# Optimization experiments

Measured on AMD Instinct MI355X. Metric: run time of the kernel, lower is better.

Reference implementation:

```python
import jax, jax.numpy as jnp
import numpy as np

GRID = 32
N = GRID * GRID
KTOP = 256          # max off-diagonal points kept per diagram (rest are diagonal, zero cost)
SINK_ITERS = 150
_idx = np.arange(N).reshape(GRID, GRID)
_EU = np.concatenate([_idx[:, :-1].ravel(), _idx[:-1, :].ravel()]).astype(np.int32)
_EV = np.concatenate([_idx[:, 1:].ravel(), _idx[1:, :].ravel()]).astype(np.int32)
E = _EU.shape[0]  # 1984 grid edges (4-connectivity, V-construction cubical complex)


def _h0_pairs(v):
    """0-dim persistence pairs of the sublevel filtration of pixel values v [N].
    Kruskal/union-find with the elder rule; trivial edges emit diagonal (w, w) pairs."""
    eu, ev = jnp.asarray(_EU), jnp.asarray(_EV)
    w = jnp.maximum(v[eu], v[ev])
    order = jnp.argsort(w)

    @jax.checkpoint
    def step(state, edge):
        parent, birth = state
        u, vv, wgt = edge
        for _ in range(10):              # pointer jumping: full compression (2^10 >= N)
            parent = parent[parent]
        ru, rv = parent[u], parent[vv]
        bu, bv = birth[ru], birth[rv]
        merge = ru != rv
        u_older = bu <= bv
        older = jnp.where(u_older, ru, rv)
        younger = jnp.where(u_older, rv, ru)
        pb = jnp.where(merge, jnp.maximum(bu, bv), wgt)   # younger component dies
        parent = parent.at[younger].set(jnp.where(merge, older, younger))
        birth = birth.at[older].set(jnp.minimum(bu, bv))
        return (parent, birth), (pb, wgt)

    init = (jnp.arange(N, dtype=jnp.int32), v)
    _, (bs, ds) = jax.lax.scan(step, init, (eu[order], ev[order], w[order]))
    return bs, ds


def _diagrams(img):
    """img [GRID,GRID] -> (b0, d0, b1, d1), each [KTOP]. H1 via superlevel H0 duality."""
    v = img.reshape(-1)
    b0, d0 = _h0_pairs(v)
    b0 = jnp.concatenate([b0, v.min()[None]])   # essential H0 class: (min, max)
    d0 = jnp.concatenate([d0, v.max()[None]])
    nb, nd = _h0_pairs(-v)                       # superlevel-set H0 (essential dropped)
    b1, d1 = -nd, -nb

    def topk(b, d):
        _, i = jax.lax.top_k(d - b, KTOP)        # keep most persistent points
        return b[i], d[i]

    return (*topk(b0, d0), *topk(b1, d1))


def _wasserstein(ab, ad, bb, bd):
    """Entropic 1-Wasserstein between diagrams with L-inf ground metric and diagonal slots."""
    K = ab.shape[0]
    Pa = jnp.stack([ab, ad], -1)
    Pb = jnp.stack([bb, bd], -1)
    Mpp = jnp.max(jnp.abs(Pa[:, None, :] - Pb[None, :, :]), -1)  # [K,K]
    da = 0.5 * (ad - ab)                       # L-inf distance of a-points to diagonal
    db = 0.5 * (bd - bb)
    C = jnp.block([[Mpp, jnp.broadcast_to(da[:, None], (K, K))],
                   [jnp.broadcast_to(db[None, :], (K, K)), jnp.zeros((K, K), ab.dtype)]])
    eps = 0.02 * jnp.maximum(jnp.max(C), 1e-6)

    def it(_, fg):
        f, g = fg
        f = -eps * jax.nn.logsumexp((g[None, :] - C) / eps, axis=1)
        g = -eps * jax.nn.logsumexp((f[:, None] - C) / eps, axis=0)
        return f, g

    f, g = jax.lax.fori_loop(0, SINK_ITERS, it, (jnp.zeros(2 * K), jnp.zeros(2 * K)))
    P = jnp.exp((f[:, None] + g[None, :] - C) / eps)
    return jnp.sum(P * C)


def setup_inputs() -> dict:
    key = jax.random.key(0)
    kx, ky = jax.random.split(key)
    x = jax.random.normal(kx, (4, 4, 256, 256), dtype=jnp.float32)
    y = jax.random.randint(ky, (4, 1, 256, 256), 0, 4)
    return {"x": x, "y": y}


def reference(x, y):
    B, C, H, W = x.shape
    x = jax.nn.softmax(x, axis=1)                               # apply_nonlin
    y_oh = (y == jnp.arange(C)[None, :, None, None]).astype(x.dtype)  # scatter_ one-hot
    kh, kw = H // GRID, W // GRID

    def pool(t):  # adaptive_avg_pool2d to (32, 32)
        b, c = t.shape[:2]
        return t.reshape(b, c, GRID, kh, GRID, kw).mean((3, 5))

    mx = pool(x[:, 1:]).reshape(-1, GRID, GRID)  # drop background channel
    my = pool(y_oh[:, 1:]).reshape(-1, GRID, GRID)
    dx = jax.vmap(_diagrams)(mx)
    dy = jax.vmap(_diagrams)(my)
    w0 = jax.vmap(_wasserstein)(dx[0], dx[1], dy[0], dy[1])
    w1 = jax.vmap(_wasserstein)(dx[2], dx[3], dy[2], dy[3])
    return (jnp.sum(w0) + jnp.sum(w1)) / B
```

## Files before the change

kernel.cpp:

```cpp
#include <hip/hip_runtime.h>
#include <cmath>

#define NPIX 1024
#define NEDGE 1984
#define NPAD 2048
#define KTOP 256
#define NITER 150

typedef __attribute__((ext_vector_type(8))) short bf16x8_t;
typedef __attribute__((ext_vector_type(4))) float f32x4_t;

__device__ __forceinline__ unsigned bf_rne(float x) {
    unsigned b = __float_as_uint(x);
    return (b + 0x7fffu + ((b >> 16) & 1u)) >> 16;
}
__device__ __forceinline__ float rcpf(float x) { return __builtin_amdgcn_rcpf(x); }

template<int CTRL>
__device__ __forceinline__ float dppf(float x) {
    return __int_as_float(__builtin_amdgcn_update_dpp(
        __float_as_int(x), __float_as_int(x), CTRL, 0xF, 0xF, false));
}
__device__ __forceinline__ void wave_red2(float& s, float& m) {
    s += dppf<0x121>(s); m = fminf(m, dppf<0x121>(m));
    s += dppf<0x122>(s); m = fminf(m, dppf<0x122>(m));
    s += dppf<0x124>(s); m = fminf(m, dppf<0x124>(m));
    s += dppf<0x128>(s); m = fminf(m, dppf<0x128>(m));
    s += __int_as_float(__builtin_amdgcn_ds_swizzle(__float_as_int(s), 0x401F));
    m = fminf(m, __int_as_float(__builtin_amdgcn_ds_swizzle(__float_as_int(m), 0x401F)));
    float s0 = __int_as_float(__builtin_amdgcn_readlane(__float_as_int(s), 0));
    float s1 = __int_as_float(__builtin_amdgcn_readlane(__float_as_int(s), 32));
    s = s0 + s1;
    float m0 = __int_as_float(__builtin_amdgcn_readlane(__float_as_int(m), 0));
    float m1 = __int_as_float(__builtin_amdgcn_readlane(__float_as_int(m), 32));
    m = fminf(m0, m1);
}

__device__ __forceinline__ float min8v(const float* a) {
    float4 x0 = *(const float4*)a, x1 = *(const float4*)(a + 4);
    return fminf(fminf(fminf(x0.x, x0.y), fminf(x0.z, x0.w)),
                 fminf(fminf(x1.x, x1.y), fminf(x1.z, x1.w)));
}
__device__ __forceinline__ float sum8v(const float* a) {
    float4 x0 = *(const float4*)a, x1 = *(const float4*)(a + 4);
    return ((x0.x + x0.y) + (x0.z + x0.w)) + ((x1.x + x1.y) + (x1.z + x1.w));
}

__global__ __launch_bounds__(256) void pool_kernel(const float* __restrict__ x,
                                                   const int* __restrict__ y,
                                                   float* __restrict__ pooled) {
    int blk = blockIdx.x;
    int img = blk >> 2;
    int cell = ((blk & 3) << 8) | threadIdx.x;
    int gi = cell >> 5, gj = cell & 31;
    const float L2E = 1.4426950408889634f;
    float acc = 0.f;
    if (img < 12) {
        int b = img / 3, c = img % 3 + 1;
        const float* xb = x + (size_t)b * 262144 + (size_t)gi * 2048 + gj * 8;
        for (int pi = 0; pi < 8; ++pi) {
            const float* xr = xb + pi * 256;
            #pragma unroll
            for (int ph = 0; ph < 2; ++ph) {
                float4 c0 = *(const float4*)(xr + ph * 4);
                float4 c1 = *(const float4*)(xr + ph * 4 + 65536);
                float4 c2 = *(const float4*)(xr + ph * 4 + 131072);
                float4 c3 = *(const float4*)(xr + ph * 4 + 196608);
                const float* f0 = (const float*)&c0;
                const float* f1 = (const float*)&c1;
                const float* f2 = (const float*)&c2;
                const float* f3 = (const float*)&c3;
                #pragma unroll
                for (int k = 0; k < 4; ++k) {
                    float e0 = exp2f(f0[k] * L2E), e1 = exp2f(f1[k] * L2E);
                    float e2 = exp2f(f2[k] * L2E), e3 = exp2f(f3[k] * L2E);
                    float ec = (c == 1) ? e1 : (c == 2) ? e2 : e3;
                    acc += ec / (e0 + e1 + e2 + e3);
                }
            }
        }
    } else {
        int tt = img - 12;
        int b = tt / 3, c = tt % 3 + 1;
        const int* yb = y + (size_t)b * 65536 + (size_t)gi * 2048 + gj * 8;
        int cnt = 0;
        for (int pi = 0; pi < 8; ++pi) {
            const int* yr = yb + pi * 256;
            #pragma unroll
            for (int pj = 0; pj < 8; ++pj) cnt += (yr[pj] == c) ? 1 : 0;
        }
        acc = (float)cnt;
    }
    pooled[img * NPIX + cell] = acc * (1.f / 64.f);
}

__device__ __forceinline__ void cex(unsigned long long& a, unsigned long long& b, bool up) {
    if ((a > b) == up) { unsigned long long t = a; a = b; b = t; }
}
__device__ void bitonic2048_reg(unsigned long long* keys, int tid, bool asc) {
    int i0 = tid << 2;
    for (int k = 2; k <= NPAD; k <<= 1) {
        for (int j = k >> 1; j >= 4; j >>= 1) {
            #pragma unroll
            for (int rep = 0; rep < 4; ++rep) {
                int ii = tid + rep * 512;
                int l = ii ^ j;
                if (l > ii) {
                    unsigned long long a = keys[ii], b = keys[l];
                    bool up = (((ii & k) == 0) == asc);
                    if ((a > b) == up) { keys[ii] = b; keys[l] = a; }
                }
            }
            __syncthreads();
        }
        unsigned long long e0 = keys[i0], e1 = keys[i0 + 1], e2 = keys[i0 + 2], e3 = keys[i0 + 3];
        bool upq = (((i0 & k) == 0) == asc);
        if (k >= 4) {
            cex(e0, e2, upq); cex(e1, e3, upq);
            cex(e0, e1, upq); cex(e2, e3, upq);
        } else {
            cex(e0, e1, asc);
            cex(e2, e3, !asc);
        }
        keys[i0] = e0; keys[i0 + 1] = e1; keys[i0 + 2] = e2; keys[i0 + 3] = e3;
        __syncthreads();
    }
}

__global__ __launch_bounds__(512) void diag_kernel(const float* __restrict__ pooled,
                                                   float* __restrict__ diag) {
    __shared__ float v_[NPIX];
    __shared__ unsigned long long keys[NPAD];
    __shared__ unsigned long long PB[NPIX];
    __shared__ unsigned euv[NPAD];
    __shared__ unsigned long long pbd[NEDGE];
    __shared__ unsigned long long snap[516];
    __shared__ unsigned long long clist[516];
    __shared__ unsigned long long smask[8];
    __shared__ unsigned claimA[NPIX];
    __shared__ unsigned histAll[2048];
    __shared__ float redA[8], redB[8];
    __shared__ float svmin, svmax;
    __shared__ unsigned long long s_prefix, s_T;
    __shared__ unsigned s_need, s_done, s_outcnt, s_ncon;

    int run = blockIdx.x;
    int img = run >> 1, filt = run & 1;
    int tid = threadIdx.x;
    int wv = tid >> 6;
    const float* m = pooled + img * NPIX;

    for (int i = tid; i < NPIX; i += 512) {
        float val = m[i];
        v_[i] = filt ? -val : val;
    }
    __syncthreads();
    float mn = INFINITY, mx = -INFINITY;
    for (int i = tid; i < NPIX; i += 512) { float vv = v_[i]; mn = fminf(mn, vv); mx = fmaxf(mx, vv); }
    for (int o = 32; o; o >>= 1) { mn = fminf(mn, __shfl_xor(mn, o)); mx = fmaxf(mx, __shfl_xor(mx, o)); }
    if ((tid & 63) == 0) { redA[wv] = mn; redB[wv] = mx; }
    __syncthreads();
    if (tid == 0) {
        float a = INFINITY, b = -INFINITY;
        for (int i2 = 0; i2 < 8; ++i2) { a = fminf(a, redA[i2]); b = fmaxf(b, redB[i2]); }
        svmin = a; svmax = b;
    }
    for (int e = tid; e < NPAD; e += 512) {
        unsigned long long key;
        unsigned uv = 0;
        if (e < NEDGE) {
            int u, vv;
            if (e < 992) { int r = e / 31; u = e + r; vv = u + 1; }
            else         { u = e - 992;   vv = u + 32; }
            float w = fmaxf(v_[u], v_[vv]);
            unsigned int bw = __float_as_uint(w);
            bw = (bw & 0x80000000u) ? ~bw : (bw | 0x80000000u);
            key = ((unsigned long long)bw << 11) | (unsigned int)e;
            uv = (unsigned)u | ((unsigned)vv << 16);
        } else key = ~0ULL;
        keys[e] = key;
        euv[e] = uv;
    }
    for (int i = tid; i < NPIX; i += 512)
        PB[i] = ((unsigned long long)__float_as_uint(v_[i]) << 32) | (unsigned)i;
    __syncthreads();
    bitonic2048_reg(keys, tid, true);

    unsigned* PBlo = (unsigned*)PB;
    for (int base = 0; base < NEDGE; base += 512) {
        for (int i = tid; i < NPIX; i += 512) claimA[i] = 0u;
        if (base) {
            for (int rd = 0; rd < 4; ++rd) {
                for (int i = tid; i < NPIX; i += 512) {
                    unsigned pp = PBlo[2 * i];
                    unsigned gg = PBlo[2 * pp];
                    PBlo[2 * i] = gg;
                }
            }
        }
        __syncthreads();
        int bend = (base + 512 < NEDGE) ? base + 512 : NEDGE;
        int bcnt = bend - base;
        bool pend = false;
        if (tid < bcnt) {
            int kk = base + tid;
            unsigned long long key = keys[kk];
            int e = (int)(key & 2047ULL);
            unsigned bw = (unsigned)(key >> 11);
            unsigned uv = euv[e];
            int ra = (int)(uv & 0xffffu), rb = (int)(uv >> 16);
            unsigned pp = PBlo[2 * ra];
            while (pp != (unsigned)ra) { ra = (int)pp; pp = PBlo[2 * ra]; }
            unsigned p2 = PBlo[2 * rb];
            while (p2 != (unsigned)rb) { rb = (int)p2; p2 = PBlo[2 * rb]; }
            if (ra == rb) {
                unsigned wb = (bw & 0x80000000u) ? (bw & 0x7fffffffu) : ~bw;
                pbd[kk] = (unsigned long long)wb | ((unsigned long long)wb << 32);
                snap[tid] = 0ULL;
            } else {
                snap[tid] = ((unsigned long long)bw << 22)
                          | ((unsigned)(ra + 1) << 11) | (unsigned)(rb + 1);
                unsigned tg = (1u << 12) | (unsigned)(511 - tid);
                atomicMax(&claimA[ra], tg);
                atomicMax(&claimA[rb], tg);
                pend = true;
            }
        }
        __syncthreads();
        for (int rnd = 0; rnd < 3; ++rnd) {
            if (pend) {
                unsigned long long sc = snap[tid];
                int ra = (int)((sc >> 11) & 0x7FFu) - 1;
                int rb = (int)(sc & 0x7FFu) - 1;
                unsigned tg = ((unsigned)(rnd + 1) << 12) | (unsigned)(511 - tid);
                if (claimA[ra] == tg && claimA[rb] == tg) {
                    unsigned ob = (unsigned)(sc >> 22);
                    float w = __uint_as_float((ob & 0x80000000u) ? (ob & 0x7fffffffu) : ~ob);
                    float bu = v_[ra], bv = v_[rb];
                    bool uo = (bu <= bv);
                    int older = uo ? ra : rb;
                    int younger = uo ? rb : ra;
                    PBlo[2 * younger] = (unsigned)older;
                    float pb_ = fmaxf(bu, bv);
                    pbd[base + tid] = (unsigned long long)__float_as_uint(pb_)
                                    | ((unsigned long long)__float_as_uint(w) << 32);
                    snap[tid] = 0ULL;
                    pend = false;
                }
            }
            __syncthreads();
            if (rnd < 2) {
                if (pend) {
                    unsigned long long sc = snap[tid];
                    int ra = (int)((sc >> 11) & 0x7FFu) - 1;
                    int rb = (int)(sc & 0x7FFu) - 1;
                    unsigned pp = PBlo[2 * ra];
                    while (pp != (unsigned)ra) { ra = (int)pp; pp = PBlo[2 * ra]; }
                    unsigned p2 = PBlo[2 * rb];
                    while (p2 != (unsigned)rb) { rb = (int)p2; p2 = PBlo[2 * rb]; }
                    if (ra == rb) {
                        unsigned ob = (unsigned)(sc >> 22);
                        unsigned wb2 = (ob & 0x80000000u) ? (ob & 0x7fffffffu) : ~ob;
                        pbd[base + tid] = (unsigned long long)wb2
                                        | ((unsigned long long)wb2 << 32);
                        snap[tid] = 0ULL;
                        pend = false;
                    } else {
                        snap[tid] = (sc & ~0x3FFFFFULL)
                                  | ((unsigned)(ra + 1) << 11) | (unsigned)(rb + 1);
                        unsigned tg = ((unsigned)(rnd + 2) << 12) | (unsigned)(511 - tid);
                        atomicMax(&claimA[ra], tg);
                        atomicMax(&claimA[rb], tg);
                    }
                }
                __syncthreads();
            }
        }
        unsigned long long bmask = __ballot(pend);
        if ((tid & 63) == 0) smask[wv] = bmask;
        __syncthreads();
        if (pend) {
            int lane = tid & 63;
            int pos = __popcll(bmask & ((1ULL << lane) - 1ULL));
            for (int w2 = 0; w2 < wv; ++w2) pos += __popcll(smask[w2]);
            clist[pos] = snap[tid] | ((unsigned long long)tid << 54);
        }
        if (tid == 0) {
            unsigned n = 0;
            for (int w2 = 0; w2 < 8; ++w2) n += (unsigned)__popcll(smask[w2]);
            s_ncon = n;
            clist[n] = 0ULL;
        }
        __syncthreads();
        if (tid == 0) {
            int n = (int)s_ncon;
            unsigned long long sc = clist[0];
            for (int i = 0; i < n; ++i) {
                unsigned long long sn = clist[i + 1];
                int slot = (int)(sc >> 54);
                unsigned ob = (unsigned)((sc >> 22) & 0xFFFFFFFFu);
                float w = __uint_as_float((ob & 0x80000000u) ? (ob & 0x7fffffffu) : ~ob);
                int a = (int)((sc >> 11) & 0x7FFu) - 1;
                int b = (int)(sc & 0x7FFu) - 1;
                unsigned long long qa = PB[a], qb = PB[b];
                int pa = (int)(unsigned)qa, pb = (int)(unsigned)qb;
                while (pa != a || pb != b) {
                    if (pa != a) {
                        unsigned long long na = PB[pa];
                        int ga = (int)(unsigned)na;
                        PBlo[2 * a] = (unsigned)ga;
                        a = pa; pa = ga; qa = na;
                    }
                    if (pb != b) {
                        unsigned long long nb = PB[pb];
                        int gb = (int)(unsigned)nb;
                        PBlo[2 * b] = (unsigned)gb;
                        b = pb; pb = gb; qb = nb;
                    }
                }
                float pb_, pd_;
                if (a != b) {
                    float bu = __uint_as_float((unsigned)(qa >> 32));
                    float bv = __uint_as_float((unsigned)(qb >> 32));
                    bool uo = (bu <= bv);
                    int older = uo ? a : b;
                    int younger = uo ? b : a;
                    pb_ = fmaxf(bu, bv); pd_ = w;
                    PBlo[2 * younger] = (unsigned)older;
                } else { pb_ = w; pd_ = w; }
                pbd[base + slot] = (unsigned long long)__float_as_uint(pb_)
                                 | ((unsigned long long)__float_as_uint(pd_) << 32);
                sc = sn;
            }
        }
        __syncthreads();
    }

    int count = filt ? NEDGE : (NEDGE + 1);
    for (int k = tid; k < NPAD; k += 512) {
        unsigned long long key = 0ULL;
        if (k < count) {
            float pers;
            if (k < NEDGE) {
                unsigned long long pd2 = pbd[k];
                pers = __uint_as_float((unsigned)(pd2 >> 32)) - __uint_as_float((unsigned)pd2);
            } else pers = svmax - svmin;
            key = ((unsigned long long)__float_as_uint(pers) << 32) | (unsigned int)(2047 - k);
        }
        keys[k] = key;
    }
    if (tid == 0) { s_prefix = 0ULL; s_T = 0ULL; s_need = KTOP; s_done = 0; s_outcnt = 0; }
    __syncthreads();

    for (int rnd = 0; rnd < 8; ++rnd) {
        for (int i = tid; i < 2048; i += 512) histAll[i] = 0;
        __syncthreads();
        if (!s_done) {
            int shift = 56 - 8 * rnd;
            unsigned long long pref = s_prefix;
            for (int k = tid; k < NPAD; k += 512) {
                unsigned long long key = keys[k];
                bool act = (rnd == 0) || ((key >> (shift + 8)) == (pref >> (shift + 8)));
                if (act) atomicAdd(&histAll[wv * 256 + (unsigned)((key >> shift) & 255ULL)], 1u);
            }
        }
        __syncthreads();
        if (wv == 0) {
            if (!s_done) {
                int l64 = tid;
                int shift = 56 - 8 * rnd;
                unsigned c0 = 0, c1 = 0, c2 = 0, c3 = 0;
                #pragma unroll
                for (int cp = 0; cp < 8; ++cp) {
                    const unsigned* h = histAll + cp * 256 + 4 * l64;
                    c0 += h[0]; c1 += h[1]; c2 += h[2]; c3 += h[3];
                }
                unsigned s3 = c3, s2 = c2 + s3, s1 = c1 + s2, s0 = c0 + s1;
                unsigned acc2 = s0;
                #pragma unroll
                for (int o = 1; o < 64; o <<= 1) {
                    unsigned v2 = __shfl_down(acc2, o);
                    if (l64 + o < 64) acc2 += v2;
                }
                unsigned above = acc2 - s0;
                unsigned Sn[5] = {above + s0, above + s1, above + s2, above + s3, above};
                unsigned need = s_need;
                #pragma unroll
                for (int q2 = 0; q2 < 4; ++q2) {
                    if (Sn[q2] >= need && Sn[q2 + 1] < need) {
                        unsigned bstar = 4 * l64 + q2;
                        if (Sn[q2] == need) {
                            s_T = s_prefix | ((unsigned long long)bstar << shift);
                            s_done = 1;
                        } else {
                            s_prefix = s_prefix | ((unsigned long long)bstar << shift);
                            s_need = need - Sn[q2 + 1];
                        }
                    }
                }
            }
        }
        __syncthreads();
    }

    {
        unsigned long long T = s_T;
        for (int k = tid; k < NPAD; k += 512) {
            unsigned long long key = keys[k];
            if (key >= T && key != 0ULL) {
                int pos = (int)atomicAdd(&s_outcnt, 1u);
                int kk = 2047 - (int)(key & 0xffffffffULL);
                float b_, d_;
                if (kk < NEDGE) {
                    unsigned long long pd2 = pbd[kk];
                    b_ = __uint_as_float((unsigned)pd2);
                    d_ = __uint_as_float((unsigned)(pd2 >> 32));
                } else { b_ = svmin; d_ = svmax; }
                float ob, od;
                if (!filt) { ob = b_;  od = d_;  }
                else       { ob = -d_; od = -b_; }
                diag[((img * 4) + filt * 2 + 0) * KTOP + pos] = ob;
                diag[((img * 4) + filt * 2 + 1) * KTOP + pos] = od;
            }
        }
    }
}

__global__ __launch_bounds__(512) void sink_kernel(const float* __restrict__ diag,
                                                   float* __restrict__ wres) {
    __shared__ float2 sPA[KTOP], sPB[KTOP];
    __shared__ float sda[KTOP], sdb[KTOP];
    __shared__ float swa[KTOP], swb[KTOP];
    __shared__ __align__(16) unsigned ug_bf[128];
    __shared__ __align__(16) unsigned uf_bf[128];
    __shared__ __align__(16) float uf32[KTOP], ug32[KTOP];
    __shared__ __align__(16) float minF[8], accTF[8], minG[8], accTG[8];
    __shared__ __align__(16) float pm[8];
    __shared__ float s_sig, s_invsig;

    int p = blockIdx.x;
    int img = p % 12, dim = p / 12;
    int t = threadIdx.x;
    int lane = t & 63, w = t >> 6;
    int lr = lane & 15, lg = lane >> 4;
    int r = t >> 1, q = t & 1, jb = q * 128;

    const float* ab  = diag + ((img * 4) + dim * 2) * KTOP;
    const float* ad  = ab + KTOP;
    const float* bbp = diag + (((12 + img) * 4) + dim * 2) * KTOP;
    const float* bdp = bbp + KTOP;

    if (t < KTOP) {
        float a0 = ab[t], a1 = ad[t];
        float b0 = bbp[t], b1 = bdp[t];
        sPA[t] = make_float2(a0, a1);
        sPB[t] = make_float2(b0, b1);
        sda[t] = 0.5f * (a1 - a0);
        sdb[t] = 0.5f * (b1 - b0);
    }
    if (t < 128) ug_bf[t] = 0x3F803F80u;
    __syncthreads();

    {
        float2 A = sPA[r];
        float lmax = 0.f;
        for (int jj = 0; jj < 128; ++jj) {
            float2 B = sPB[jb + jj];
            lmax = fmaxf(lmax, fmaxf(fabsf(A.x - B.x), fabsf(A.y - B.y)));
        }
        if (t < KTOP) lmax = fmaxf(lmax, fmaxf(sda[t], sdb[t]));
        for (int o = 32; o; o >>= 1) lmax = fmaxf(lmax, __shfl_xor(lmax, o));
        if (lane == 0) pm[w] = lmax;
    }
    __syncthreads();
    if (t == 0) {
        float mc = 0.f;
        for (int i = 0; i < 8; ++i) mc = fmaxf(mc, pm[i]);
        float eps = 0.02f * fmaxf(mc, 1e-6f);
        s_sig = 1.4426950408889634f / eps;
        s_invsig = eps * 0.6931471805599453f;
    }
    __syncthreads();
    {
        float sig = s_sig;
        if (t < KTOP) {
            float2 a2 = sPA[t], b2 = sPB[t];
            sPA[t] = make_float2(a2.x * sig, a2.y * sig);
            sPB[t] = make_float2(b2.x * sig, b2.y * sig);
            float da2 = sda[t] * sig, db2 = sdb[t] * sig;
            sda[t] = da2; sdb[t] = db2;
            swa[t] = exp2f(-da2); swb[t] = exp2f(-db2);
        }
    }
    __syncthreads();

    bf16x8_t KfA0[8], KfA1[8], KgA0[8], KgA1[8];
    {
        float2 Af0 = sPA[w * 32 + lr];
        float2 Af1 = sPA[w * 32 + 16 + lr];
        float2 Bg0 = sPB[w * 32 + lr];
        float2 Bg1 = sPB[w * 32 + 16 + lr];
        #pragma unroll
        for (int ks = 0; ks < 8; ++ks) {
            #pragma unroll
            for (int jj = 0; jj < 8; ++jj) {
                int b = ks * 32 + lg * 8 + jj;
                float2 Pb = sPB[b];
                KfA0[ks][jj] = (short)bf_rne(exp2f(-fmaxf(fabsf(Af0.x - Pb.x), fabsf(Af0.y - Pb.y))));
                KfA1[ks][jj] = (short)bf_rne(exp2f(-fmaxf(fabsf(Af1.x - Pb.x), fabsf(Af1.y - Pb.y))));
                float2 Pa = sPA[b];
                KgA0[ks][jj] = (short)bf_rne(exp2f(-fmaxf(fabsf(Pa.x - Bg0.x), fabsf(Pa.y - Bg0.y))));
                KgA1[ks][jj] = (short)bf_rne(exp2f(-fmaxf(fabsf(Pa.x - Bg1.x), fabsf(Pa.y - Bg1.y))));
            }
        }
    }
    float wa0[4], wa1[4], wb0[4], wb1[4];
    #pragma unroll
    for (int g2 = 0; g2 < 4; ++g2) {
        wa0[g2] = swa[w * 32 + lg * 4 + g2];
        wa1[g2] = swa[w * 32 + 16 + lg * 4 + g2];
        wb0[g2] = swb[w * 32 + lg * 4 + g2];
        wb1[g2] = swb[w * 32 + 16 + lg * 4 + g2];
    }

    float cg = 1.f, cf = 1.f, uG2s = 1.f, uF2s = 1.f;
    f32x4_t ugs0 = {1.f, 1.f, 1.f, 1.f}, ugs1 = {1.f, 1.f, 1.f, 1.f};
    f32x4_t ufs0 = {0.f, 0.f, 0.f, 0.f}, ufs1 = {0.f, 0.f, 0.f, 0.f};

    for (int it = 0; it < NITER; ++it) {
        if (it) {
            cg = min8v(minG);
            uG2s = rcpf(cf * (sum8v(accTG) + 256.f * uF2s));
        }
        {
            bf16x8_t Bf[8];
            #pragma unroll
            for (int ks = 0; ks < 8; ++ks) Bf[ks] = ((const bf16x8_t*)ug_bf)[ks * 4 + lg];
            f32x4_t a0 = {0.f, 0.f, 0.f, 0.f}, a1 = {0.f, 0.f, 0.f, 0.f};
            f32x4_t c0 = {0.f, 0.f, 0.f, 0.f}, c1 = {0.f, 0.f, 0.f, 0.f};
            #pragma unroll
            for (int ks = 0; ks < 4; ++ks) {
                a0 = __builtin_amdgcn_mfma_f32_16x16x32_bf16(KfA0[ks], Bf[ks], a0, 0, 0, 0);
                a1 = __builtin_amdgcn_mfma_f32_16x16x32_bf16(KfA1[ks], Bf[ks], a1, 0, 0, 0);
                c0 = __builtin_amdgcn_mfma_f32_16x16x32_bf16(KfA0[ks + 4], Bf[ks + 4], c0, 0, 0, 0);
                c1 = __builtin_amdgcn_mfma_f32_16x16x32_bf16(KfA1[ks + 4], Bf[ks + 4], c1, 0, 0, 0);
            }
            a0 = a0 + c0;
            a1 = a1 + c1;
            float mv = INFINITY, tv = 0.f;
            #pragma unroll
            for (int g2 = 0; g2 < 4; ++g2) {
                float R0 = cg * (a0[g2] + 256.f * uG2s * wa0[g2]);
                float R1 = cg * (a1[g2] + 256.f * uG2s * wa1[g2]);
                ufs0[g2] = rcpf(R0); ufs1[g2] = rcpf(R1);
                mv = fminf(mv, fminf(R0, R1));
                tv += ugs0[g2] * wb0[g2] + ugs1[g2] * wb1[g2];
            }
            if (lr == 0) {
                uint2 v0, v1;
                v0.x = bf_rne(ufs0[0]) | (bf_rne(ufs0[1]) << 16);
                v0.y = bf_rne(ufs0[2]) | (bf_rne(ufs0[3]) << 16);
                v1.x = bf_rne(ufs1[0]) | (bf_rne(ufs1[1]) << 16);
                v1.y = bf_rne(ufs1[2]) | (bf_rne(ufs1[3]) << 16);
                ((uint2*)uf_bf)[w * 8 + lg] = v0;
                ((uint2*)uf_bf)[w * 8 + 4 + lg] = v1;
            }
            wave_red2(tv, mv);
            if (lane == 0) { accTF[w] = tv * 0.0625f; minF[w] = mv; }
        }
        __syncthreads();
        cf = min8v(minF);
        uF2s = rcpf(cg * (sum8v(accTF) + 256.f * uG2s));
        {
            bf16x8_t Bf[8];
            #pragma unroll
            for (int ks = 0; ks < 8; ++ks) Bf[ks] = ((const bf16x8_t*)uf_bf)[ks * 4 + lg];
            f32x4_t a0 = {0.f, 0.f, 0.f, 0.f}, a1 = {0.f, 0.f, 0.f, 0.f};
            f32x4_t c0 = {0.f, 0.f, 0.f, 0.f}, c1 = {0.f, 0.f, 0.f, 0.f};
            #pragma unroll
            for (int ks = 0; ks < 4; ++ks) {
                a0 = __builtin_amdgcn_mfma_f32_16x16x32_bf16(KgA0[ks], Bf[ks], a0, 0, 0, 0);
                a1 = __builtin_amdgcn_mfma_f32_16x16x32_bf16(KgA1[ks], Bf[ks], a1, 0, 0, 0);
                c0 = __builtin_amdgcn_mfma_f32_16x16x32_bf16(KgA0[ks + 4], Bf[ks + 4], c0, 0, 0, 0);
                c1 = __builtin_amdgcn_mfma_f32_16x16x32_bf16(KgA1[ks + 4], Bf[ks + 4], c1, 0, 0, 0);
            }
            a0 = a0 + c0;
            a1 = a1 + c1;
            float mv = INFINITY, tv = 0.f;
            #pragma unroll
            for (int g2 = 0; g2 < 4; ++g2) {
                float Q0 = cf * (a0[g2] + 256.f * uF2s * wb0[g2]);
                float Q1 = cf * (a1[g2] + 256.f * uF2s * wb1[g2]);
                ugs0[g2] = rcpf(Q0); ugs1[g2] = rcpf(Q1);
                mv = fminf(mv, fminf(Q0, Q1));
                tv += ufs0[g2] * wa0[g2] + ufs1[g2] * wa1[g2];
            }
            if (lr == 0) {
                uint2 v0, v1;
                v0.x = bf_rne(ugs0[0]) | (bf_rne(ugs0[1]) << 16);
                v0.y = bf_rne(ugs0[2]) | (bf_rne(ugs0[3]) << 16);
                v1.x = bf_rne(ugs1[0]) | (bf_rne(ugs1[1]) << 16);
                v1.y = bf_rne(ugs1[2]) | (bf_rne(ugs1[3]) << 16);
                ((uint2*)ug_bf)[w * 8 + lg] = v0;
                ((uint2*)ug_bf)[w * 8 + 4 + lg] = v1;
            }
            wave_red2(tv, mv);
            if (lane == 0) { accTG[w] = tv * 0.0625f; minG[w] = mv; }
        }
        __syncthreads();
    }
    float uG2f = rcpf(cf * (sum8v(accTG) + 256.f * uF2s));
    if (lr == 0) {
        ((f32x4_t*)uf32)[w * 8 + lg] = ufs0;
        ((f32x4_t*)uf32)[w * 8 + 4 + lg] = ufs1;
        ((f32x4_t*)ug32)[w * 8 + lg] = ugs0;
        ((f32x4_t*)ug32)[w * 8 + 4 + lg] = ugs1;
    }
    __syncthreads();

    float accv = 0.f;
    {
        float2 Apt = sPA[r];
        float ufr = uf32[r];
        #pragma unroll 8
        for (int jj = 0; jj < 128; ++jj) {
            int j = jb + jj;
            float2 B = sPB[j];
            float Mh = fmaxf(fabsf(Apt.x - B.x), fabsf(Apt.y - B.y));
            float kv = __uint_as_float(bf_rne(exp2f(-Mh)) << 16);
            accv += ((ufr * kv) * ug32[j]) * Mh;
        }
        if (q == 0) accv += 256.f * ((ufr * swa[r]) * uG2f) * sda[r];
        else        accv += 256.f * ((uF2s * swb[r]) * ug32[r]) * sdb[r];
    }
    accv *= cf;
    for (int o = 32; o; o >>= 1) accv += __shfl_xor(accv, o);
    if (lane == 0) pm[w] = accv;
    __syncthreads();
    if (t == 0) {
        float tot = 0.f;
        for (int i = 0; i < 8; ++i) tot += pm[i];
        wres[p] = tot * s_invsig;
    }
}

__global__ void finalize_kernel(const float* __restrict__ wres, float* __restrict__ out) {
    if (threadIdx.x == 0) {
        float s = 0.f;
        for (int i = 0; i < 24; ++i) s += wres[i];
        out[0] = s * 0.25f;
    }
}

extern "C" void kernel_launch(void* const* d_in, const int* in_sizes, int n_in,
                              void* d_out, int out_size, void* d_ws, size_t ws_size,
                              hipStream_t stream) {
    const float* x = (const float*)d_in[0];
    const int* y = (const int*)d_in[1];
    float* ws = (float*)d_ws;
    float* pooled = ws;
    float* diag = pooled + 24 * NPIX;
    float* wres = diag + 24 * 4 * KTOP;

    pool_kernel<<<96, 256, 0, stream>>>(x, y, pooled);
    diag_kernel<<<48, 512, 0, stream>>>(pooled, diag);
    sink_kernel<<<24, 512, 0, stream>>>(diag, wres);
    finalize_kernel<<<1, 64, 0, stream>>>(wres, (float*)d_out);
}
```

Measured before the change: 764.6 us.

## Fuse pooling into diag kernel and finalize into sink via atomic counter

The separate pooling kernel is removed: each diag block now computes the softmax-pooled or one-hot-pooled 32x32 image itself, straight from the inputs. The finalize kernel is replaced by a last-block-done atomic counter in the sink kernel, and the radix-select loop now breaks early once the threshold is found. This cuts two kernel launches and the round trip through the pooled buffer. In exchange, each of the two filtration blocks per image recomputes the same pooling, and correctness depends on the counter being reset in diag_kernel before sink_kernel runs.

Measured after the change: 789.8 us (median of 2 runs). 3.3% more time.

```diff
diff --git a/kernel.cpp b/kernel.cpp
--- a/kernel.cpp
+++ b/kernel.cpp
@@ -46,54 +46,6 @@
     return ((x0.x + x0.y) + (x0.z + x0.w)) + ((x1.x + x1.y) + (x1.z + x1.w));
 }
 
-__global__ __launch_bounds__(256) void pool_kernel(const float* __restrict__ x,
-                                                   const int* __restrict__ y,
-                                                   float* __restrict__ pooled) {
-    int blk = blockIdx.x;
-    int img = blk >> 2;
-    int cell = ((blk & 3) << 8) | threadIdx.x;
-    int gi = cell >> 5, gj = cell & 31;
-    const float L2E = 1.4426950408889634f;
-    float acc = 0.f;
-    if (img < 12) {
-        int b = img / 3, c = img % 3 + 1;
-        const float* xb = x + (size_t)b * 262144 + (size_t)gi * 2048 + gj * 8;
-        for (int pi = 0; pi < 8; ++pi) {
-            const float* xr = xb + pi * 256;
-            #pragma unroll
-            for (int ph = 0; ph < 2; ++ph) {
-                float4 c0 = *(const float4*)(xr + ph * 4);
-                float4 c1 = *(const float4*)(xr + ph * 4 + 65536);
-                float4 c2 = *(const float4*)(xr + ph * 4 + 131072);
-                float4 c3 = *(const float4*)(xr + ph * 4 + 196608);
-                const float* f0 = (const float*)&c0;
-                const float* f1 = (const float*)&c1;
-                const float* f2 = (const float*)&c2;
-                const float* f3 = (const float*)&c3;
-                #pragma unroll
-                for (int k = 0; k < 4; ++k) {
-                    float e0 = exp2f(f0[k] * L2E), e1 = exp2f(f1[k] * L2E);
-                    float e2 = exp2f(f2[k] * L2E), e3 = exp2f(f3[k] * L2E);
-                    float ec = (c == 1) ? e1 : (c == 2) ? e2 : e3;
-                    acc += ec / (e0 + e1 + e2 + e3);
-                }
-            }
-        }
-    } else {
-        int tt = img - 12;
-        int b = tt / 3, c = tt % 3 + 1;
-        const int* yb = y + (size_t)b * 65536 + (size_t)gi * 2048 + gj * 8;
-        int cnt = 0;
-        for (int pi = 0; pi < 8; ++pi) {
-            const int* yr = yb + pi * 256;
-            #pragma unroll
-            for (int pj = 0; pj < 8; ++pj) cnt += (yr[pj] == c) ? 1 : 0;
-        }
-        acc = (float)cnt;
-    }
-    pooled[img * NPIX + cell] = acc * (1.f / 64.f);
-}
-
 __device__ __forceinline__ void cex(unsigned long long& a, unsigned long long& b, bool up) {
     if ((a > b) == up) { unsigned long long t = a; a = b; b = t; }
 }
@@ -127,8 +79,10 @@
     }
 }
 
-__global__ __launch_bounds__(512) void diag_kernel(const float* __restrict__ pooled,
-                                                   float* __restrict__ diag) {
+__global__ __launch_bounds__(512) void diag_kernel(const float* __restrict__ x,
+                                                   const int* __restrict__ y,
+                                                   float* __restrict__ diag,
+                                                   unsigned* __restrict__ cnt) {
     __shared__ float v_[NPIX];
     __shared__ unsigned long long keys[NPAD];
     __shared__ unsigned long long PB[NPIX];
@@ -148,11 +102,51 @@
     int img = run >> 1, filt = run & 1;
     int tid = threadIdx.x;
     int wv = tid >> 6;
-    const float* m = pooled + img * NPIX;
-
-    for (int i = tid; i < NPIX; i += 512) {
-        float val = m[i];
-        v_[i] = filt ? -val : val;
+
+    if (run == 0 && tid == 0) *cnt = 0;
+
+    const float L2E = 1.4426950408889634f;
+    for (int cell = tid; cell < NPIX; cell += 512) {
+        int gi = cell >> 5, gj = cell & 31;
+        float acc = 0.f;
+        if (img < 12) {
+            int b = img / 3, c = img % 3 + 1;
+            const float* xb = x + (size_t)b * 262144 + (size_t)gi * 2048 + gj * 8;
+            for (int pi = 0; pi < 8; ++pi) {
+                const float* xr = xb + pi * 256;
+                #pragma unroll
+                for (int ph = 0; ph < 2; ++ph) {
+                    float4 c0 = *(const float4*)(xr + ph * 4);
+                    float4 c1 = *(const float4*)(xr + ph * 4 + 65536);
+                    float4 c2 = *(const float4*)(xr + ph * 4 + 131072);
+                    float4 c3 = *(const float4*)(xr + ph * 4 + 196608);
+                    const float* f0 = (const float*)&c0;
+                    const float* f1 = (const float*)&c1;
+                    const float* f2 = (const float*)&c2;
+                    const float* f3 = (const float*)&c3;
+                    #pragma unroll
+                    for (int k = 0; k < 4; ++k) {
+                        float e0 = exp2f(f0[k] * L2E), e1 = exp2f(f1[k] * L2E);
+                        float e2 = exp2f(f2[k] * L2E), e3 = exp2f(f3[k] * L2E);
+                        float ec = (c == 1) ? e1 : (c == 2) ? e2 : e3;
+                        acc += ec / (e0 + e1 + e2 + e3);
+                    }
+                }
+            }
+        } else {
+            int tt = img - 12;
+            int b = tt / 3, c = tt % 3 + 1;
+            const int* yb = y + (size_t)b * 65536 + (size_t)gi * 2048 + gj * 8;
+            int cn = 0;
+            for (int pi = 0; pi < 8; ++pi) {
+                const int* yr = yb + pi * 256;
+                #pragma unroll
+                for (int pj = 0; pj < 8; ++pj) cn += (yr[pj] == c) ? 1 : 0;
+            }
+            acc = (float)cn;
+        }
+        float val = acc * (1.f / 64.f);
+        v_[cell] = filt ? -val : val;
     }
     __syncthreads();
     float mn = INFINITY, mx = -INFINITY;
@@ -355,7 +349,7 @@
     for (int rnd = 0; rnd < 8; ++rnd) {
         for (int i = tid; i < 2048; i += 512) histAll[i] = 0;
         __syncthreads();
-        if (!s_done) {
+        {
             int shift = 56 - 8 * rnd;
             unsigned long long pref = s_prefix;
             for (int k = tid; k < NPAD; k += 512) {
@@ -366,41 +360,40 @@
         }
         __syncthreads();
         if (wv == 0) {
-            if (!s_done) {
-                int l64 = tid;
-                int shift = 56 - 8 * rnd;
-                unsigned c0 = 0, c1 = 0, c2 = 0, c3 = 0;
-                #pragma unroll
-                for (int cp = 0; cp < 8; ++cp) {
-                    const unsigned* h = histAll + cp * 256 + 4 * l64;
-                    c0 += h[0]; c1 += h[1]; c2 += h[2]; c3 += h[3];
-                }
-                unsigned s3 = c3, s2 = c2 + s3, s1 = c1 + s2, s0 = c0 + s1;
-                unsigned acc2 = s0;
-                #pragma unroll
-                for (int o = 1; o < 64; o <<= 1) {
-                    unsigned v2 = __shfl_down(acc2, o);
-                    if (l64 + o < 64) acc2 += v2;
-                }
-                unsigned above = acc2 - s0;
-                unsigned Sn[5] = {above + s0, above + s1, above + s2, above + s3, above};
-                unsigned need = s_need;
-                #pragma unroll
-                for (int q2 = 0; q2 < 4; ++q2) {
-                    if (Sn[q2] >= need && Sn[q2 + 1] < need) {
-                        unsigned bstar = 4 * l64 + q2;
-                        if (Sn[q2] == need) {
-                            s_T = s_prefix | ((unsigned long long)bstar << shift);
-                            s_done = 1;
-                        } else {
-                            s_prefix = s_prefix | ((unsigned long long)bstar << shift);
-                            s_need = need - Sn[q2 + 1];
-                        }
+            int l64 = tid;
+            int shift = 56 - 8 * rnd;
+            unsigned c0 = 0, c1 = 0, c2 = 0, c3 = 0;
+            #pragma unroll
+            for (int cp = 0; cp < 8; ++cp) {
+                const unsigned* h = histAll + cp * 256 + 4 * l64;
+                c0 += h[0]; c1 += h[1]; c2 += h[2]; c3 += h[3];
+            }
+            unsigned s3 = c3, s2 = c2 + s3, s1 = c1 + s2, s0 = c0 + s1;
+            unsigned acc2 = s0;
+            #pragma unroll
+            for (int o = 1; o < 64; o <<= 1) {
+                unsigned v2 = __shfl_down(acc2, o);
+                if (l64 + o < 64) acc2 += v2;
+            }
+            unsigned above = acc2 - s0;
+            unsigned Sn[5] = {above + s0, above + s1, above + s2, above + s3, above};
+            unsigned need = s_need;
+            #pragma unroll
+            for (int q2 = 0; q2 < 4; ++q2) {
+                if (Sn[q2] >= need && Sn[q2 + 1] < need) {
+                    unsigned bstar = 4 * l64 + q2;
+                    if (Sn[q2] == need) {
+                        s_T = s_prefix | ((unsigned long long)bstar << shift);
+                        s_done = 1;
+                    } else {
+                        s_prefix = s_prefix | ((unsigned long long)bstar << shift);
+                        s_need = need - Sn[q2 + 1];
                     }
                 }
             }
         }
         __syncthreads();
+        if (s_done) break;
     }
 
     {
@@ -427,7 +420,9 @@
 }
 
 __global__ __launch_bounds__(512) void sink_kernel(const float* __restrict__ diag,
-                                                   float* __restrict__ wres) {
+                                                   float* __restrict__ wres,
+                                                   unsigned* __restrict__ cnt,
+                                                   float* __restrict__ out) {
     __shared__ float2 sPA[KTOP], sPB[KTOP];
     __shared__ float sda[KTOP], sdb[KTOP];
     __shared__ float swa[KTOP], swb[KTOP];
@@ -641,14 +636,13 @@
         float tot = 0.f;
         for (int i = 0; i < 8; ++i) tot += pm[i];
         wres[p] = tot * s_invsig;
-    }
-}
-
-__global__ void finalize_kernel(const float* __restrict__ wres, float* __restrict__ out) {
-    if (threadIdx.x == 0) {
-        float s = 0.f;
-        for (int i = 0; i < 24; ++i) s += wres[i];
-        out[0] = s * 0.25f;
+        __threadfence();
+        unsigned old = atomicAdd(cnt, 1u);
+        if (old == 23) {
+            float s = 0.f;
+            for (int i = 0; i < 24; ++i) s += atomicAdd(&wres[i], 0.0f);
+            out[0] = s * 0.25f;
+        }
     }
 }
 
@@ -658,12 +652,10 @@
     const float* x = (const float*)d_in[0];
     const int* y = (const int*)d_in[1];
     float* ws = (float*)d_ws;
-    float* pooled = ws;
-    float* diag = pooled + 24 * NPIX;
+    float* diag = ws;
     float* wres = diag + 24 * 4 * KTOP;
-
-    pool_kernel<<<96, 256, 0, stream>>>(x, y, pooled);
-    diag_kernel<<<48, 512, 0, stream>>>(pooled, diag);
-    sink_kernel<<<24, 512, 0, stream>>>(diag, wres);
-    finalize_kernel<<<1, 64, 0, stream>>>(wres, (float*)d_out);
-}
+    unsigned* cnt = (unsigned*)(wres + 24);
+
+    diag_kernel<<<48, 512, 0, stream>>>(x, y, diag, cnt);
+    sink_kernel<<<24, 512, 0, stream>>>(diag, wres, cnt, (float*)d_out);
+}
```
